# Kernel tuning notes

Measured on AMD Instinct MI355X. Metric: run time of the kernel, lower is better.

## Reference

```python
import jax, jax.numpy as jnp
import numpy as np

B, N, D, H = 2, 2048, 1024, 16
DK = D // H
SCALE = DK ** -0.5


def setup_inputs() -> dict:
    key = jax.random.key(0)
    ks = jax.random.split(key, 11)
    s = D ** -0.5
    return {
        "q": jax.random.normal(ks[0], (B, N, D), jnp.float32),
        "k": jax.random.normal(ks[1], (B, N, D), jnp.float32),
        "v": jax.random.normal(ks[2], (B, N, D), jnp.float32),
        "Wq": jax.random.normal(ks[3], (D, D), jnp.float32) * s,
        "bq": jnp.zeros((D,), jnp.float32),
        "Wk": jax.random.normal(ks[4], (D, D), jnp.float32) * s,
        "bk": jnp.zeros((D,), jnp.float32),
        "Wv": jax.random.normal(ks[5], (D, D), jnp.float32) * s,
        "bv": jnp.zeros((D,), jnp.float32),
        "Wo": jax.random.normal(ks[6], (D, D), jnp.float32) * s,
        "bo": jnp.zeros((D,), jnp.float32),
    }


def _split_heads(x):
    # [b, n, h*d] -> [b, h, n, d]
    b, n, _ = x.shape
    return x.reshape(b, n, H, DK).transpose(0, 2, 1, 3)


def reference(q, k, v, Wq, bq, Wk, bk, Wv, bv, Wo, bo):
    qh = _split_heads(q @ Wq.T + bq)
    kh = _split_heads(k @ Wk.T + bk)
    vh = _split_heads(v @ Wv.T + bv)
    dots = jnp.einsum('bhid,bhjd->bhij', qh, kh) * SCALE
    attn = jax.nn.softmax(dots, axis=-1)
    out = jnp.einsum('bhij,bhjd->bhid', attn, vh)
    out = out.transpose(0, 2, 1, 3).reshape(q.shape[0], q.shape[1], D)
    return out @ Wo.T + bo
```

## Files before the change

### kernel.cpp

```cpp
#include <hip/hip_runtime.h>
#include <hip/hip_bf16.h>
#include <cstdint>
#include <cstddef>

#define BB 2
#define NN 2048
#define DD 1024
#define HH 16
#define DKK 64
#define SCALE 0.125f
#define LOG2E 1.4426950408889634f

typedef __bf16 bf16;
typedef __bf16 bf16x4 __attribute__((ext_vector_type(4)));
typedef __bf16 bf16x8 __attribute__((ext_vector_type(8)));
typedef float f32x4 __attribute__((ext_vector_type(4)));
typedef short s16x4 __attribute__((ext_vector_type(4)));

#define GLD(gp, lp)                                                            \
  __builtin_amdgcn_global_load_lds(                                            \
      (const __attribute__((address_space(1))) void*)(gp),                     \
      (__attribute__((address_space(3))) void*)(lp), 16, 0, 0)

struct CvtArgs { const float* s[7]; bf16* d[7]; int n[7]; };

__global__ void k_cvt(CvtArgs a) {
  const int seg = blockIdx.y;
  const float* __restrict__ s = a.s[seg];
  bf16* __restrict__ d = a.d[seg];
  int i = (blockIdx.x * 256 + threadIdx.x) * 8;
  if (i >= a.n[seg]) return;
  float4 f0 = *(const float4*)(s + i);
  float4 f1 = *(const float4*)(s + i + 4);
  bf16x8 o;
  o[0] = (bf16)f0.x; o[1] = (bf16)f0.y; o[2] = (bf16)f0.z; o[3] = (bf16)f0.w;
  o[4] = (bf16)f1.x; o[5] = (bf16)f1.y; o[6] = (bf16)f1.z; o[7] = (bf16)f1.w;
  *(bf16x8*)(d + i) = o;
}

template <int BN>
__device__ __forceinline__ void gemm_body(
    const bf16* __restrict__ A, const bf16* __restrict__ W,
    const float* __restrict__ bias, bf16* __restrict__ outB,
    float* __restrict__ outF, int mode, float oscale, int m0, int n0) {
  const int K = 1024;
  constexpr int NI = BN / 32;
  constexpr int BI = BN * 8 / 256;
  __shared__ bf16 lA[128 * 64];
  __shared__ bf16 lB[BN * 64];
  const int t = threadIdx.x;
  const int lane = t & 63, quad = lane >> 4, l16 = lane & 15, w = t >> 6;
  const int wm = (w >> 1) * 64, wn = (w & 1) * (BN / 2);

  f32x4 acc[4][NI] = {};

  const bf16* gA[4]; const bf16* gB[BI];
#pragma unroll
  for (int i4 = 0; i4 < 4; i4++) {
    int i = i4 * 256 + t;
    int r = i >> 3, c = (i & 7) ^ (r & 7);
    gA[i4] = A + (size_t)(m0 + r) * K + c * 8;
  }
#pragma unroll
  for (int i4 = 0; i4 < BI; i4++) {
    int i = i4 * 256 + t;
    int r = i >> 3, c = (i & 7) ^ (r & 7);
    gB[i4] = W + (size_t)(n0 + r) * K + c * 8;
  }

  for (int kb = 0; kb < K; kb += 64) {
    __syncthreads();
#pragma unroll
    for (int i4 = 0; i4 < 4; i4++) GLD(gA[i4] + kb, lA + (i4 * 256 + t) * 8);
#pragma unroll
    for (int i4 = 0; i4 < BI; i4++) GLD(gB[i4] + kb, lB + (i4 * 256 + t) * 8);
    __syncthreads();

#pragma unroll
    for (int kb2 = 0; kb2 < 2; kb2++) {
      bf16x8 af[4], bfr[NI];
      const int ch = ((kb2 * 4 + quad) ^ (l16 & 7)) * 8;
#pragma unroll
      for (int i = 0; i < 4; i++)
        af[i] = *(const bf16x8*)(lA + (wm + i * 16 + l16) * 64 + ch);
#pragma unroll
      for (int i = 0; i < NI; i++)
        bfr[i] = *(const bf16x8*)(lB + (wn + i * 16 + l16) * 64 + ch);
#pragma unroll
      for (int mi = 0; mi < 4; mi++)
#pragma unroll
        for (int ni = 0; ni < NI; ni++)
          acc[mi][ni] = __builtin_amdgcn_mfma_f32_16x16x32_bf16(
              af[mi], bfr[ni], acc[mi][ni], 0, 0, 0);
    }
  }

  if (mode == 2) {
    __syncthreads();
    bf16* scr = (w < 2 ? lA : lB) + (w & 1) * 4096;
#pragma unroll
    for (int ni = 0; ni < NI; ni++) {
      int c = ni * 16 + l16;
      float bs = bias[n0 + wn + c];
#pragma unroll
      for (int mi = 0; mi < 4; mi++) {
        int u = (mi * 2 + (quad >> 1)) ^ (c & 7);
        bf16x4 pv;
#pragma unroll
        for (int r = 0; r < 4; r++)
          pv[r] = (bf16)((acc[mi][ni][r] + bs) * oscale);
        *(bf16x4*)(scr + c * 64 + u * 8 + (quad & 1) * 4) = pv;
      }
    }
    __syncthreads();
    {
      const int gm0 = m0 + wm;
      const int b = gm0 >> 11, row0 = gm0 & 2047;
#pragma unroll
      for (int it = 0; it < 8; it++) {
        int c = it * 8 + (lane >> 3);
        int u = (lane & 7) ^ (lane >> 3);
        bf16x8 val = *(const bf16x8*)(scr + c * 64 + u * 8);
        int gn = n0 + wn + c;
        int h = gn >> 6, dk = gn & 63;
        *(bf16x8*)(outB + ((size_t)(b * HH + h) * DKK + dk) * NN + row0 +
                   (lane & 7) * 8) = val;
      }
    }
    return;
  }
#pragma unroll
  for (int mi = 0; mi < 4; mi++) {
#pragma unroll
    for (int ni = 0; ni < NI; ni++) {
#pragma unroll
      for (int r = 0; r < 4; r++) {
        int gm = m0 + wm + mi * 16 + quad * 4 + r;
        int gn = n0 + wn + ni * 16 + l16;
        float v = (acc[mi][ni][r] + bias[gn]) * oscale;
        if (mode == 3) {
          outF[(size_t)gm * 1024 + gn] = v;
        } else {
          int b = gm >> 11, row = gm & 2047;
          int h = gn >> 6, dk = gn & 63;
          outB[((size_t)(b * HH + h) * NN + row) * DKK + dk] = (bf16)v;
        }
      }
    }
  }
}

struct QkvArgs {
  const bf16* A; const bf16* W; const float* b[3]; bf16* o[3]; float sc0;
};

__global__ __launch_bounds__(256, 3) void k_qkv(QkvArgs g) {
  const int z = blockIdx.z;
  gemm_body<128>(g.A + (size_t)z * 4194304, g.W + (size_t)z * 1048576,
                 g.b[z], g.o[z], nullptr, z == 2 ? 2 : 0,
                 z == 0 ? g.sc0 : 1.0f, blockIdx.x * 128, blockIdx.y * 128);
}

__global__ __launch_bounds__(256, 4) void k_oproj(
    const bf16* __restrict__ A, const bf16* __restrict__ W,
    const float* __restrict__ bias, float* __restrict__ out) {
  gemm_body<64>(A, W, bias, nullptr, out, 3, 1.0f, blockIdx.x * 128,
                blockIdx.y * 64);
}

__global__ __launch_bounds__(512, 4) void k_attn(
    const bf16* __restrict__ Qp, const bf16* __restrict__ Kp,
    const bf16* __restrict__ Vt, bf16* __restrict__ Ao) {
  __shared__ bf16 lKV[2][8192];
  __shared__ float redL2[512];
  const int t = threadIdx.x;
  const int lane = t & 63, quad = lane >> 4, l16 = lane & 15, w = t >> 6;
  const int wq = w & 3;
  const int kh = w >> 2;
  const int bh = blockIdx.x;
  const int qt = blockIdx.y;
  const bf16* Qb = Qp + (size_t)bh * NN * DKK;
  const bf16* Kb = Kp + (size_t)bh * NN * DKK;
  const bf16* Vb = Vt + (size_t)bh * DKK * NN;

  const int qr0 = qt * 128 + wq * 32;
  bf16x8 qf[2][2];
#pragma unroll
  for (int j = 0; j < 2; j++)
#pragma unroll
    for (int kq = 0; kq < 2; kq++)
      qf[j][kq] = *(const bf16x8*)(Qb + (size_t)(qr0 + j * 16 + l16) * DKK +
                                   kq * 32 + quad * 8);

  float lj[2] = {0.f, 0.f};
  f32x4 oaccT[2][4] = {};

  const int rS = t >> 3, cS = (t & 7) ^ (rS & 7);
  const bf16* gK = Kb + (size_t)rS * DKK + cS * 8;
  const bf16* gV = Vb + (size_t)rS * NN + cS * 8;
  const int swzK0 = (quad ^ (l16 & 7)) * 8;
  const int swzK1 = ((4 + quad) ^ (l16 & 7)) * 8;

  GLD(gK, &lKV[0][t * 8]);
  GLD(gV, &lKV[0][4096 + t * 8]);

  int p = 0;
  for (int kt = 0; kt < NN; kt += 64) {
    __syncthreads();
    if (kt + 64 < NN) {
      GLD(gK + (size_t)(kt + 64) * DKK, &lKV[p ^ 1][t * 8]);
      GLD(gV + (kt + 64), &lKV[p ^ 1][4096 + t * 8]);
    }

    f32x4 s[2][2];
#pragma unroll
    for (int tt = 0; tt < 2; tt++) {
      const bf16* kbase = &lKV[p][((kh * 2 + tt) * 16 + l16) * 64];
      bf16x8 kf0 = *(const bf16x8*)(kbase + swzK0);
      bf16x8 kf1 = *(const bf16x8*)(kbase + swzK1);
#pragma unroll
      for (int j = 0; j < 2; j++) {
        f32x4 z = {0.f, 0.f, 0.f, 0.f};
        z = __builtin_amdgcn_mfma_f32_16x16x32_bf16(kf0, qf[j][0], z, 0, 0, 0);
        z = __builtin_amdgcn_mfma_f32_16x16x32_bf16(kf1, qf[j][1], z, 0, 0, 0);
        s[j][tt] = z;
      }
    }

    s16x4 pa[2][2];
#pragma unroll
    for (int j = 0; j < 2; j++) {
      float rs = 0.f;
#pragma unroll
      for (int tt = 0; tt < 2; tt++) {
        bf16x4 pb;
#pragma unroll
        for (int r = 0; r < 4; r++) {
          float pe = __builtin_amdgcn_exp2f(s[j][tt][r]);
          rs += pe;
          pb[r] = (bf16)pe;
        }
        pa[j][tt] = __builtin_bit_cast(s16x4, pb);
      }
      lj[j] += rs;
    }

#pragma unroll
    for (int tt = 0; tt < 2; tt++) {
#pragma unroll
      for (int ni = 0; ni < 4; ni++) {
        int rv = ni * 16 + l16;
        int u = kh * 4 + 2 * tt + (quad >> 1);
        const bf16* vaddr =
            &lKV[p][4096 + rv * 64 + ((u ^ (l16 & 7)) * 8) + (quad & 1) * 4];
        s16x4 vb = __builtin_bit_cast(s16x4, *(const bf16x4*)vaddr);
#pragma unroll
        for (int j = 0; j < 2; j++)
          oaccT[j][ni] = __builtin_amdgcn_mfma_f32_16x16x16bf16_1k(
              vb, pa[j][tt], oaccT[j][ni], 0, 0, 0);
      }
    }
    p ^= 1;
  }

  __syncthreads();
  float* redO = (float*)&lKV[0][0];
  const int R = wq * 64 + lane;
  if (kh == 1) {
#pragma unroll
    for (int j = 0; j < 2; j++)
#pragma unroll
      for (int ni = 0; ni < 4; ni++)
        *(f32x4*)(redO + ((j * 4 + ni) * 1024 + R * 4)) = oaccT[j][ni];
    redL2[R * 2 + 0] = lj[0];
    redL2[R * 2 + 1] = lj[1];
  }
  __syncthreads();
  if (kh == 0) {
#pragma unroll
    for (int j = 0; j < 2; j++)
#pragma unroll
      for (int ni = 0; ni < 4; ni++)
        oaccT[j][ni] += *(const f32x4*)(redO + ((j * 4 + ni) * 1024 + R * 4));
    lj[0] += redL2[R * 2 + 0];
    lj[1] += redL2[R * 2 + 1];

    const int b = bh >> 4, h = bh & 15;
#pragma unroll
    for (int j = 0; j < 2; j++) {
      float l = lj[j];
      l += __shfl_xor(l, 16);
      l += __shfl_xor(l, 32);
      const float inv = 1.0f / l;
      bf16* dst = Ao + ((size_t)(b * NN) + qr0 + j * 16 + l16) * DD +
                  h * DKK + quad * 4;
#pragma unroll
      for (int ni = 0; ni < 4; ni++) {
        bf16x4 ov;
#pragma unroll
        for (int r = 0; r < 4; r++) ov[r] = (bf16)(oaccT[j][ni][r] * inv);
        *(bf16x4*)(dst + ni * 16) = ov;
      }
    }
  }
}

extern "C" void kernel_launch(void* const* d_in, const int* in_sizes, int n_in,
                              void* d_out, int out_size, void* d_ws,
                              size_t ws_size, hipStream_t stream) {
  const float* qin = (const float*)d_in[0];
  const float* kin = (const float*)d_in[1];
  const float* vin = (const float*)d_in[2];
  const float* Wq = (const float*)d_in[3];
  const float* bq = (const float*)d_in[4];
  const float* Wk = (const float*)d_in[5];
  const float* bk = (const float*)d_in[6];
  const float* Wv = (const float*)d_in[7];
  const float* bv = (const float*)d_in[8];
  const float* Wo = (const float*)d_in[9];
  const float* bo = (const float*)d_in[10];
  float* out = (float*)d_out;

  const int MN = BB * NN * DD;
  const int WNel = DD * DD;
  bf16* ws = (bf16*)d_ws;
  bf16* Xb = ws;
  bf16* Wb = Xb + 3 * MN;
  bf16* Qp = Wb + 4 * WNel;
  bf16* Kp = Qp + MN;
  bf16* Vt = Kp + MN;
  bf16* Ao = Xb;

  CvtArgs ca{{qin, kin, vin, Wq, Wk, Wv, Wo},
             {Xb, Xb + MN, Xb + 2 * MN, Wb, Wb + WNel, Wb + 2 * WNel,
              Wb + 3 * WNel},
             {MN, MN, MN, WNel, WNel, WNel, WNel}};
  k_cvt<<<dim3(2048, 7), 256, 0, stream>>>(ca);

  QkvArgs g{Xb, Wb, {bq, bk, bv}, {Qp, Kp, Vt}, SCALE * LOG2E};
  k_qkv<<<dim3(32, 8, 3), 256, 0, stream>>>(g);
  k_attn<<<dim3(32, 16), 512, 0, stream>>>(Qp, Kp, Vt, Ao);
  k_oproj<<<dim3(32, 16), 256, 0, stream>>>(Ao, Wb + 3 * WNel, bo, out);
}
```

Measured before the change: 207.1 us.

## Fuse fp32-to-bf16 activation conversion into QKV GEMM tile loads

The separate conversion pass over the q/k/v activations is removed. The QKV GEMM now loads fp32 activation tiles directly, converts them to bf16 in registers and stores them to LDS, so only the weights still go through the conversion kernel. This cuts a full write and re-read of three bf16 activation buffers. In exchange the A-tile loads become synchronous register loads instead of async global-to-LDS loads, which adds register pressure and latency, and each activation element is read and converted once per N-tile block.

```diff
diff --git a/kernel.cpp b/kernel.cpp
--- a/kernel.cpp
+++ b/kernel.cpp
@@ -22,7 +22,7 @@
       (const __attribute__((address_space(1))) void*)(gp),                     \
       (__attribute__((address_space(3))) void*)(lp), 16, 0, 0)
 
-struct CvtArgs { const float* s[7]; bf16* d[7]; int n[7]; };
+struct CvtArgs { const float* s[4]; bf16* d[4]; int n[4]; };
 
 __global__ void k_cvt(CvtArgs a) {
   const int seg = blockIdx.y;
@@ -38,11 +38,12 @@
   *(bf16x8*)(d + i) = o;
 }
 
-template <int BN>
+template <int BN, bool AF32>
 __device__ __forceinline__ void gemm_body(
-    const bf16* __restrict__ A, const bf16* __restrict__ W,
-    const float* __restrict__ bias, bf16* __restrict__ outB,
-    float* __restrict__ outF, int mode, float oscale, int m0, int n0) {
+    const bf16* __restrict__ A, const float* __restrict__ A32,
+    const bf16* __restrict__ W, const float* __restrict__ bias,
+    bf16* __restrict__ outB, float* __restrict__ outF, int mode, float oscale,
+    int m0, int n0) {
   const int K = 1024;
   constexpr int NI = BN / 32;
   constexpr int BI = BN * 8 / 256;
@@ -54,12 +55,15 @@
 
   f32x4 acc[4][NI] = {};
 
-  const bf16* gA[4]; const bf16* gB[BI];
+  const bf16* gA[4]; const float* gA32[4]; const bf16* gB[BI];
 #pragma unroll
   for (int i4 = 0; i4 < 4; i4++) {
     int i = i4 * 256 + t;
     int r = i >> 3, c = (i & 7) ^ (r & 7);
-    gA[i4] = A + (size_t)(m0 + r) * K + c * 8;
+    if constexpr (AF32)
+      gA32[i4] = A32 + (size_t)(m0 + r) * K + c * 8;
+    else
+      gA[i4] = A + (size_t)(m0 + r) * K + c * 8;
   }
 #pragma unroll
   for (int i4 = 0; i4 < BI; i4++) {
@@ -71,9 +75,27 @@
   for (int kb = 0; kb < K; kb += 64) {
     __syncthreads();
 #pragma unroll
-    for (int i4 = 0; i4 < 4; i4++) GLD(gA[i4] + kb, lA + (i4 * 256 + t) * 8);
-#pragma unroll
     for (int i4 = 0; i4 < BI; i4++) GLD(gB[i4] + kb, lB + (i4 * 256 + t) * 8);
+    if constexpr (AF32) {
+      f32x4 a0[4], a1[4];
+#pragma unroll
+      for (int i4 = 0; i4 < 4; i4++) {
+        a0[i4] = *(const f32x4*)(gA32[i4] + kb);
+        a1[i4] = *(const f32x4*)(gA32[i4] + kb + 4);
+      }
+#pragma unroll
+      for (int i4 = 0; i4 < 4; i4++) {
+        bf16x8 o;
+        o[0] = (bf16)a0[i4][0]; o[1] = (bf16)a0[i4][1];
+        o[2] = (bf16)a0[i4][2]; o[3] = (bf16)a0[i4][3];
+        o[4] = (bf16)a1[i4][0]; o[5] = (bf16)a1[i4][1];
+        o[6] = (bf16)a1[i4][2]; o[7] = (bf16)a1[i4][3];
+        *(bf16x8*)(lA + (i4 * 256 + t) * 8) = o;
+      }
+    } else {
+#pragma unroll
+      for (int i4 = 0; i4 < 4; i4++) GLD(gA[i4] + kb, lA + (i4 * 256 + t) * 8);
+    }
     __syncthreads();
 
 #pragma unroll
@@ -151,21 +173,22 @@
 }
 
 struct QkvArgs {
-  const bf16* A; const bf16* W; const float* b[3]; bf16* o[3]; float sc0;
+  const float* A32[3]; const bf16* W; const float* b[3]; bf16* o[3]; float sc0;
 };
 
 __global__ __launch_bounds__(256, 3) void k_qkv(QkvArgs g) {
   const int z = blockIdx.z;
-  gemm_body<128>(g.A + (size_t)z * 4194304, g.W + (size_t)z * 1048576,
-                 g.b[z], g.o[z], nullptr, z == 2 ? 2 : 0,
-                 z == 0 ? g.sc0 : 1.0f, blockIdx.x * 128, blockIdx.y * 128);
+  gemm_body<128, true>(nullptr, g.A32[z], g.W + (size_t)z * 1048576, g.b[z],
+                       g.o[z], nullptr, z == 2 ? 2 : 0,
+                       z == 0 ? g.sc0 : 1.0f, blockIdx.x * 128,
+                       blockIdx.y * 128);
 }
 
 __global__ __launch_bounds__(256, 4) void k_oproj(
     const bf16* __restrict__ A, const bf16* __restrict__ W,
     const float* __restrict__ bias, float* __restrict__ out) {
-  gemm_body<64>(A, W, bias, nullptr, out, 3, 1.0f, blockIdx.x * 128,
-                blockIdx.y * 64);
+  gemm_body<64, false>(A, nullptr, W, bias, nullptr, out, 3, 1.0f,
+                       blockIdx.x * 128, blockIdx.y * 64);
 }
 
 __global__ __launch_bounds__(512, 4) void k_attn(
@@ -324,20 +347,18 @@
   const int MN = BB * NN * DD;
   const int WNel = DD * DD;
   bf16* ws = (bf16*)d_ws;
-  bf16* Xb = ws;
-  bf16* Wb = Xb + 3 * MN;
+  bf16* Wb = ws;
   bf16* Qp = Wb + 4 * WNel;
   bf16* Kp = Qp + MN;
   bf16* Vt = Kp + MN;
-  bf16* Ao = Xb;
-
-  CvtArgs ca{{qin, kin, vin, Wq, Wk, Wv, Wo},
-             {Xb, Xb + MN, Xb + 2 * MN, Wb, Wb + WNel, Wb + 2 * WNel,
-              Wb + 3 * WNel},
-             {MN, MN, MN, WNel, WNel, WNel, WNel}};
-  k_cvt<<<dim3(2048, 7), 256, 0, stream>>>(ca);
-
-  QkvArgs g{Xb, Wb, {bq, bk, bv}, {Qp, Kp, Vt}, SCALE * LOG2E};
+  bf16* Ao = Vt + MN;
+
+  CvtArgs ca{{Wq, Wk, Wv, Wo},
+             {Wb, Wb + WNel, Wb + 2 * WNel, Wb + 3 * WNel},
+             {WNel, WNel, WNel, WNel}};
+  k_cvt<<<dim3(512, 4), 256, 0, stream>>>(ca);
+
+  QkvArgs g{{qin, kin, vin}, Wb, {bq, bk, bv}, {Qp, Kp, Vt}, SCALE * LOG2E};
   k_qkv<<<dim3(32, 8, 3), 256, 0, stream>>>(g);
   k_attn<<<dim3(32, 16), 512, 0, stream>>>(Qp, Kp, Vt, Ao);
   k_oproj<<<dim3(32, 16), 256, 0, stream>>>(Ao, Wb + 3 * WNel, bo, out);
```

Result: slower. 217.8 us (+5.2%).
